# Kernel tuning notes

Hardware: AMD Instinct MI355X
Metric: run time of the kernel (lower is better)

The kernel has to match this reference:

```python
import jax, jax.numpy as jnp
import numpy as np

N_HEAD, F_IN, F_OUT = 4, 768, 64
BS, N = 4, 2048


def setup_inputs() -> dict:
    key = jax.random.key(0)
    k_h, k_w, k_src, k_dst = jax.random.split(key, 4)
    # xavier_uniform bounds
    lim_w = float(np.sqrt(6.0 / (F_IN + F_OUT)))
    lim_a = float(np.sqrt(6.0 / (F_OUT + 1)))
    return {
        "h": jax.random.normal(k_h, (BS, N, F_IN), dtype=jnp.float32),
        "w": jax.random.uniform(k_w, (N_HEAD, F_IN, F_OUT), jnp.float32, -lim_w, lim_w),
        "a_src": jax.random.uniform(k_src, (N_HEAD, F_OUT, 1), jnp.float32, -lim_a, lim_a),
        "a_dst": jax.random.uniform(k_dst, (N_HEAD, F_OUT, 1), jnp.float32, -lim_a, lim_a),
        "bias": jnp.zeros((F_OUT,), dtype=jnp.float32),
    }


def reference(h, w, a_src, a_dst, bias):
    # h: [b, n, f_in]; w: [h, f_in, f_out]
    h_prime = jnp.einsum("bnf,hfo->bhno", h, w)          # [b, h, n, f_out]
    t = jnp.tanh(h_prime)
    attn_src = jnp.einsum("bhno,ho->bhn", t, a_src[..., 0])  # [b, h, n]
    attn_dst = jnp.einsum("bhno,ho->bhn", t, a_dst[..., 0])  # [b, h, n]
    # broadcast add: attn[b,h,i,j] = src[b,h,i] + dst[b,h,j]
    attn = attn_src[..., :, None] + attn_dst[..., None, :]   # [b, h, n, n]
    attn = jnp.where(attn >= 0, attn, 0.2 * attn)            # leaky_relu(0.2)
    attn = jax.nn.softmax(attn, axis=-1)
    out = jnp.einsum("bhij,bhjo->bhio", attn, h_prime)       # [b, h, n, f_out]
    return out + bias
```

## Files before the change

### kernel.cpp

```cpp
#include <hip/hip_runtime.h>
#include <hip/hip_bf16.h>

#define NHEAD 4
#define FIN   768
#define FOUT  64
#define BSZ   4
#define NSEQ  2048
#define BH    (BSZ*NHEAD)
#define LOG2E 1.44269504088896f

typedef __attribute__((ext_vector_type(8)))  short bf16x8;
typedef __attribute__((ext_vector_type(16))) float f32x16;
typedef __attribute__((ext_vector_type(8)))  unsigned short u16x8;
typedef __attribute__((ext_vector_type(4)))  unsigned short u16x4;
typedef __attribute__((ext_vector_type(4)))  unsigned u32x4;

__device__ __forceinline__ unsigned short f2bf(float f){
  unsigned b = __float_as_uint(f);
  return (unsigned short)((b + 0x7fffu + ((b >> 16) & 1u)) >> 16);
}
__device__ __forceinline__ unsigned fenc(float f){
  unsigned b = __float_as_uint(f);
  return (b & 0x80000000u) ? ~b : (b | 0x80000000u);
}
__device__ __forceinline__ float fdec(unsigned u){
  unsigned b = (u & 0x80000000u) ? (u ^ 0x80000000u) : ~u;
  return __uint_as_float(b);
}
__device__ __forceinline__ float fexp2(float x){
#if __has_builtin(__builtin_amdgcn_exp2f)
  return __builtin_amdgcn_exp2f(x);
#else
  return exp2f(x);
#endif
}
__device__ __forceinline__ unsigned pkbf(float lo, float hi){
#if __has_builtin(__builtin_amdgcn_cvt_pk_bf16_f32)
  typedef __attribute__((ext_vector_type(2))) __bf16 bf2;
  union { bf2 v; unsigned u; } cv;
  cv.v = __builtin_amdgcn_cvt_pk_bf16_f32(lo, hi);
  return cv.u;
#else
  return (unsigned)f2bf(lo) | ((unsigned)f2bf(hi) << 16);
#endif
}

__global__ __launch_bounds__(256) void k_prep_w(
    const float* __restrict__ w, unsigned short* __restrict__ wp,
    unsigned* __restrict__ dmaxe)
{
  if (blockIdx.x == 0 && blockIdx.y == 0 && threadIdx.x < BH)
    dmaxe[threadIdx.x] = 0;
  const int head = blockIdx.x, kt = blockIdx.y;
  #pragma unroll
  for (int p = 0; p < 2; ++p){
    int u = threadIdx.x + p*256;
    int o = u >> 3, c = u & 7;
    u16x8 pk;
    #pragma unroll
    for (int j = 0; j < 8; ++j)
      pk[j] = f2bf(w[((size_t)head*FIN + kt*64 + c*8 + j)*FOUT + o]);
    *(u16x8*)((char*)wp + ((size_t)((head*12 + kt)*64 + o))*128 + c*16) = pk;
  }
}

__global__ __launch_bounds__(512, 4) void k_hprime(
    const float* __restrict__ h, const unsigned short* __restrict__ wp,
    const float* __restrict__ a_src, const float* __restrict__ a_dst,
    unsigned short* __restrict__ hpz2, float* __restrict__ srcv,
    float* __restrict__ dstv, unsigned* __restrict__ dmaxe)
{
  __shared__ __align__(16) char smem[32768];
  float* psumS = (float*)(smem + 24576);
  float* psumD = (float*)(smem + 25088);
  char*  Tt    = smem + 16384;

  const int tid  = threadIdx.x;
  const int i0a  = blockIdx.x * 64;
  const int jbase = i0a & (NSEQ-1);
  const int head = blockIdx.y;
  const int wave = tid >> 6, lane = tid & 63;
  const int wm = wave & 1, wn = (wave >> 1) & 1, kw = wave >> 2;
  const int l32 = lane & 31, h32 = lane >> 5;

  f32x16 acc = {0,0,0,0,0,0,0,0,0,0,0,0,0,0,0,0};

  const int sr = tid >> 3, sc = tid & 7;
  const float* hA = h + (size_t)(i0a + sr)*FIN + sc*8;
  const char* wrow = (const char*)wp
      + ((size_t)(head*12*64) + wn*32 + l32)*128 + h32*16;
  const int aslot = (sc ^ (sr & 7)) << 4;

  float4 ra0 = *(const float4*)(hA);
  float4 ra1 = *(const float4*)(hA + 4);
  float4 ra2 = *(const float4*)(hA + 64);
  float4 ra3 = *(const float4*)(hA + 68);

  for (int it = 0; it < 6; ++it){
    char* Ab = smem + (it & 1)*16384;
    u32x4 pk0, pk1;
    pk0[0] = pkbf(ra0.x, ra0.y); pk0[1] = pkbf(ra0.z, ra0.w);
    pk0[2] = pkbf(ra1.x, ra1.y); pk0[3] = pkbf(ra1.z, ra1.w);
    pk1[0] = pkbf(ra2.x, ra2.y); pk1[1] = pkbf(ra2.z, ra2.w);
    pk1[2] = pkbf(ra3.x, ra3.y); pk1[3] = pkbf(ra3.z, ra3.w);
    *(u32x4*)(Ab + sr*256 + aslot)       = pk0;
    *(u32x4*)(Ab + sr*256 + 128 + aslot) = pk1;
    __syncthreads();
    if (it < 5){
      const float* an = hA + (it+1)*128;
      ra0 = *(const float4*)(an);      ra1 = *(const float4*)(an + 4);
      ra2 = *(const float4*)(an + 64); ra3 = *(const float4*)(an + 68);
    }
    const char* wpan = wrow + (size_t)(2*it + kw)*8192;
    bf16x8 b0 = *(const bf16x8*)(wpan);
    bf16x8 b1 = *(const bf16x8*)(wpan + 32);
    bf16x8 b2 = *(const bf16x8*)(wpan + 64);
    bf16x8 b3 = *(const bf16x8*)(wpan + 96);
    const char* abase = Ab + (wm*32 + l32)*256 + kw*128;
    bf16x8 a0 = *(const bf16x8*)(abase + (((0 + h32) ^ (l32 & 7)) << 4));
    bf16x8 a1 = *(const bf16x8*)(abase + (((2 + h32) ^ (l32 & 7)) << 4));
    bf16x8 a2 = *(const bf16x8*)(abase + (((4 + h32) ^ (l32 & 7)) << 4));
    bf16x8 a3 = *(const bf16x8*)(abase + (((6 + h32) ^ (l32 & 7)) << 4));
    acc = __builtin_amdgcn_mfma_f32_32x32x16_bf16(a0, b0, acc, 0, 0, 0);
    acc = __builtin_amdgcn_mfma_f32_32x32x16_bf16(a1, b1, acc, 0, 0, 0);
    acc = __builtin_amdgcn_mfma_f32_32x32x16_bf16(a2, b2, acc, 0, 0, 0);
    acc = __builtin_amdgcn_mfma_f32_32x32x16_bf16(a3, b3, acc, 0, 0, 0);
  }

  if (kw == 1) *(f32x16*)(smem + (size_t)((wave & 3)*64 + lane)*64) = acc;
  __syncthreads();
  if (kw == 0){
    acc += *(const f32x16*)(smem + (size_t)((wave & 3)*64 + lane)*64);
    const float as = a_src[head*64 + wn*32 + l32];
    const float ad = a_dst[head*64 + wn*32 + l32];
    #pragma unroll
    for (int rb = 0; rb < 4; ++rb){
      const int jb = wm*32 + rb*8 + h32*4;
      u16x4 c4;
      #pragma unroll
      for (int q = 0; q < 4; ++q){
        const float v = acc[rb*4 + q];
        c4[q] = f2bf(v);
        const float t = tanhf(v);
        float ps = t*as, pd = t*ad;
        ps += __shfl_xor(ps, 1);  ps += __shfl_xor(ps, 2);  ps += __shfl_xor(ps, 4);
        ps += __shfl_xor(ps, 8);  ps += __shfl_xor(ps, 16);
        pd += __shfl_xor(pd, 1);  pd += __shfl_xor(pd, 2);  pd += __shfl_xor(pd, 4);
        pd += __shfl_xor(pd, 8);  pd += __shfl_xor(pd, 16);
        if (l32 == 0){
          psumS[(jb + q)*2 + wn] = ps;
          psumD[(jb + q)*2 + wn] = pd;
        }
      }
      const int orow = wn*32 + l32;
      const int slot = ((jb >> 3) & 7) ^ (orow & 7);
      *(u16x4*)(Tt + orow*128 + slot*16 + (jb & 7)*2) = c4;
    }
  }
  __syncthreads();

  const int bh = (i0a >> 11)*NHEAD + head;
  {
    const int o = tid & 63, c = tid >> 6;
    u16x8 val = *(const u16x8*)(Tt + o*128 + ((c ^ (o & 7)) << 4));
    *(u16x8*)((char*)hpz2 + ((size_t)(bh*256 + (jbase >> 3) + c)*64 + o)*16) = val;
  }
  if (tid < 64){
    float sv = (psumS[tid*2] + psumS[tid*2 + 1]) * LOG2E;
    float dv = (psumD[tid*2] + psumD[tid*2 + 1]) * LOG2E;
    srcv[(size_t)bh*NSEQ + jbase + tid] = sv;
    dstv[(size_t)bh*NSEQ + jbase + tid] = dv;
    float dmx = dv;
    dmx = fmaxf(dmx, __shfl_xor(dmx, 1));  dmx = fmaxf(dmx, __shfl_xor(dmx, 2));
    dmx = fmaxf(dmx, __shfl_xor(dmx, 4));  dmx = fmaxf(dmx, __shfl_xor(dmx, 8));
    dmx = fmaxf(dmx, __shfl_xor(dmx, 16)); dmx = fmaxf(dmx, __shfl_xor(dmx, 32));
    if (tid == 0) atomicMax(&dmaxe[bh], fenc(dmx));
  }
}

__global__ __launch_bounds__(512, 6) void k_attn(
    const unsigned short* __restrict__ hpz2, const float* __restrict__ srcv,
    const float* __restrict__ dstv, const unsigned* __restrict__ dmaxe,
    const float* __restrict__ bias, float* __restrict__ out)
{
  __shared__ __align__(16) char smem[33792];
  float* Lbuf = (float*)(smem + 32768);

  const int tid = threadIdx.x;
  const int i0  = blockIdx.x * 64;
  const int bh  = blockIdx.y;
  const int wave = tid >> 6, lane = tid & 63;
  const int wm = wave & 1, jw = wave >> 1;
  const int l32 = lane & 31, h32 = lane >> 5;

  const float s2  = srcv[(size_t)bh*NSEQ + i0 + wm*32 + l32];
  const float dm2 = fdec(dmaxe[bh]);
  float m2 = s2 + dm2; m2 = fmaxf(m2, 0.2f*m2);
  const float u_ = s2 - m2;
  const float v_ = 0.2f*s2 - m2;
  const float* dst = dstv + (size_t)bh*NSEQ;

  const u16x8* gp = (const u16x8*)((const char*)hpz2 + (size_t)bh*256*64*16);

  f32x16 accO0 = {0,0,0,0,0,0,0,0,0,0,0,0,0,0,0,0};
  f32x16 accO1 = {0,0,0,0,0,0,0,0,0,0,0,0,0,0,0,0};
  float lpart = 0.f;

  *(u16x8*)(smem + tid*16)              = gp[tid];
  *(u16x8*)(smem + (tid + 512)*16)      = gp[tid + 512];
  __syncthreads();

  for (int w = 0; w < 16; ++w){
    char* cur = smem + (w & 1)*16384;
    char* nxt = smem + ((w + 1) & 1)*16384;
    u16x8 r0, r1;
    if (w < 15){
      r0 = gp[(w+1)*1024 + tid];
      r1 = gp[(w+1)*1024 + tid + 512];
    }
    #pragma unroll
    for (int stl = 0; stl < 2; ++stl){
      const int Jl = jw*4 + stl*2 + h32;
      const int j0 = (w*16 + Jl)*8;
      float4 d0 = *(const float4*)(dst + j0);
      float4 d1 = *(const float4*)(dst + j0 + 4);
      float e0,e1,e2,e3,e4,e5,e6,e7;
      e0 = fexp2(fmaxf(u_ + d0.x, fmaf(0.2f, d0.x, v_)));
      e1 = fexp2(fmaxf(u_ + d0.y, fmaf(0.2f, d0.y, v_)));
      e2 = fexp2(fmaxf(u_ + d0.z, fmaf(0.2f, d0.z, v_)));
      e3 = fexp2(fmaxf(u_ + d0.w, fmaf(0.2f, d0.w, v_)));
      e4 = fexp2(fmaxf(u_ + d1.x, fmaf(0.2f, d1.x, v_)));
      e5 = fexp2(fmaxf(u_ + d1.y, fmaf(0.2f, d1.y, v_)));
      e6 = fexp2(fmaxf(u_ + d1.z, fmaf(0.2f, d1.z, v_)));
      e7 = fexp2(fmaxf(u_ + d1.w, fmaf(0.2f, d1.w, v_)));
      lpart += ((e0+e1)+(e2+e3)) + ((e4+e5)+(e6+e7));
      u32x4 pk;
      pk[0] = pkbf(e0, e1); pk[1] = pkbf(e2, e3);
      pk[2] = pkbf(e4, e5); pk[3] = pkbf(e6, e7);
      const bf16x8 pA = __builtin_bit_cast(bf16x8, pk);
      const bf16x8 bv0 = *(const bf16x8*)(cur + (Jl*64 +      l32)*16);
      const bf16x8 bv1 = *(const bf16x8*)(cur + (Jl*64 + 32 + l32)*16);
      accO0 = __builtin_amdgcn_mfma_f32_32x32x16_bf16(pA, bv0, accO0, 0, 0, 0);
      accO1 = __builtin_amdgcn_mfma_f32_32x32x16_bf16(pA, bv1, accO1, 0, 0, 0);
    }
    if (w < 15){
      *(u16x8*)(nxt + tid*16)         = r0;
      *(u16x8*)(nxt + (tid + 512)*16) = r1;
    }
    __syncthreads();
  }

  lpart += __shfl_xor(lpart, 32);
  if (lane < 32) Lbuf[(wm*4 + jw)*32 + l32] = lpart;

  const float4 bia = *(const float4*)(bias + (tid & 15)*4);
  #pragma unroll
  for (int ph = 0; ph < 2; ++ph){
    __syncthreads();
    if (wm == ph){
      float* ob = (float*)smem;
      #pragma unroll
      for (int reg = 0; reg < 16; ++reg){
        const int m = (reg & 3) + 8*(reg >> 2) + 4*h32;
        ob[(jw*32 + m)*64 +      l32] = accO0[reg];
        ob[(jw*32 + m)*64 + 32 + l32] = accO1[reg];
      }
    }
    __syncthreads();
    {
      const int i = tid >> 4, o4 = (tid & 15)*4;
      const float* ob = (const float*)smem;
      float4 v0 = *(const float4*)(ob + (0*32 + i)*64 + o4);
      float4 v1 = *(const float4*)(ob + (1*32 + i)*64 + o4);
      float4 v2 = *(const float4*)(ob + (2*32 + i)*64 + o4);
      float4 v3 = *(const float4*)(ob + (3*32 + i)*64 + o4);
      const float l = Lbuf[(ph*4+0)*32 + i] + Lbuf[(ph*4+1)*32 + i]
                    + Lbuf[(ph*4+2)*32 + i] + Lbuf[(ph*4+3)*32 + i];
      const float r = 1.f / l;
      float4 res;
      res.x = (v0.x + v1.x + v2.x + v3.x)*r + bia.x;
      res.y = (v0.y + v1.y + v2.y + v3.y)*r + bia.y;
      res.z = (v0.z + v1.z + v2.z + v3.z)*r + bia.z;
      res.w = (v0.w + v1.w + v2.w + v3.w)*r + bia.w;
      *(float4*)(out + ((size_t)bh*NSEQ + i0 + ph*32 + i)*64 + o4) = res;
    }
  }
}

extern "C" void kernel_launch(void* const* d_in, const int* in_sizes, int n_in,
                              void* d_out, int out_size, void* d_ws, size_t ws_size,
                              hipStream_t stream)
{
  const float* h     = (const float*)d_in[0];
  const float* w     = (const float*)d_in[1];
  const float* a_src = (const float*)d_in[2];
  const float* a_dst = (const float*)d_in[3];
  const float* bias  = (const float*)d_in[4];
  float* out = (float*)d_out;

  char* ws = (char*)d_ws;
  unsigned short* hpz2 = (unsigned short*)ws;
  float* srcv = (float*)(ws + (4u<<20));
  float* dstv = (float*)(ws + (4u<<20) + (128u<<10));
  unsigned short* wp = (unsigned short*)(ws + (4u<<20) + (256u<<10));
  unsigned* dmaxe = (unsigned*)(ws + (4u<<20) + (640u<<10));

  k_prep_w<<<dim3(NHEAD, 12), 256, 0, stream>>>(w, wp, dmaxe);
  k_hprime<<<dim3(NSEQ*BSZ/64, NHEAD), 512, 0, stream>>>(h, wp, a_src, a_dst,
                                                         hpz2, srcv, dstv, dmaxe);
  k_attn<<<dim3(NSEQ/64, BH), 512, 0, stream>>>(hpz2, srcv, dstv, dmaxe, bias, out);
}
```

Measured before the change: 134.4 us.

## Fuse three kernels into one persistent launch with atomic-counter dependencies

Replaces the weight-prep, h_prime and attention kernels with a single 512-block kernel. Blocks first pack weights, signal per-head counters, then compute their h_prime tile and signal per-batch-head counters before spinning to start the attention phase. The h_prime stage now stages W tiles through LDS instead of reading them per lane from global memory. This removes two kernel launch gaps, but adds spin-wait latency, a memset launch, and a deadlock risk if not all 512 blocks are co-resident. The guarded spin would then time out and read incomplete data.

```diff
diff --git a/kernel.cpp b/kernel.cpp
--- a/kernel.cpp
+++ b/kernel.cpp
@@ -44,245 +44,253 @@
   return (unsigned)f2bf(lo) | ((unsigned)f2bf(hi) << 16);
 #endif
 }
-
-__global__ __launch_bounds__(256) void k_prep_w(
-    const float* __restrict__ w, unsigned short* __restrict__ wp,
-    unsigned* __restrict__ dmaxe)
+__device__ __forceinline__ void spin_until(unsigned* p, unsigned target){
+  int guard = 0;
+  while (__hip_atomic_load(p, __ATOMIC_ACQUIRE, __HIP_MEMORY_SCOPE_AGENT) != target
+         && ++guard < (1 << 22))
+    __builtin_amdgcn_s_sleep(2);
+}
+
+__global__ __launch_bounds__(512, 4) void k_fused(
+    const float* __restrict__ h, const float* __restrict__ w,
+    const float* __restrict__ a_src, const float* __restrict__ a_dst,
+    const float* __restrict__ bias, float* __restrict__ out,
+    unsigned short* __restrict__ wp, unsigned short* __restrict__ hpz2,
+    float* __restrict__ srcv, float* __restrict__ dstv,
+    unsigned* __restrict__ dmaxe, unsigned* __restrict__ wcnt,
+    unsigned* __restrict__ bhcnt)
 {
-  if (blockIdx.x == 0 && blockIdx.y == 0 && threadIdx.x < BH)
-    dmaxe[threadIdx.x] = 0;
-  const int head = blockIdx.x, kt = blockIdx.y;
-  #pragma unroll
-  for (int p = 0; p < 2; ++p){
-    int u = threadIdx.x + p*256;
-    int o = u >> 3, c = u & 7;
+  __shared__ __align__(16) char smem[65536];
+  const int tid = threadIdx.x;
+  const int bx  = blockIdx.x;
+  const int wave = tid >> 6, lane = tid & 63;
+  const int l32 = lane & 31, h32 = lane >> 5;
+
+  if (bx < 48){
+    const int head = bx / 12, kt = bx - head*12;
+    const int o = tid & 63, c = (tid >> 6) & 7;
+    const float* wsrc = w + (size_t)head*FIN*FOUT + (size_t)(kt*64 + c*8)*FOUT + o;
     u16x8 pk;
     #pragma unroll
-    for (int j = 0; j < 8; ++j)
-      pk[j] = f2bf(w[((size_t)head*FIN + kt*64 + c*8 + j)*FOUT + o]);
-    *(u16x8*)((char*)wp + ((size_t)((head*12 + kt)*64 + o))*128 + c*16) = pk;
+    for (int j = 0; j < 8; ++j) pk[j] = f2bf(wsrc[(size_t)j*FOUT]);
+    *(u16x8*)((char*)wp + ((size_t)((head*12 + kt)*64 + o))*128 + ((c ^ (o & 7)) << 4)) = pk;
+    __threadfence();
+    __syncthreads();
+    if (tid == 0) atomicAdd(&wcnt[head], 1u);
   }
-}
-
-__global__ __launch_bounds__(512, 4) void k_hprime(
-    const float* __restrict__ h, const unsigned short* __restrict__ wp,
-    const float* __restrict__ a_src, const float* __restrict__ a_dst,
-    unsigned short* __restrict__ hpz2, float* __restrict__ srcv,
-    float* __restrict__ dstv, unsigned* __restrict__ dmaxe)
-{
-  __shared__ __align__(16) char smem[32768];
-  float* psumS = (float*)(smem + 24576);
-  float* psumD = (float*)(smem + 25088);
-  char*  Tt    = smem + 16384;
-
-  const int tid  = threadIdx.x;
-  const int i0a  = blockIdx.x * 64;
+
+  const int head1 = bx & 3;
+  const int i0a   = (bx >> 2) << 6;
   const int jbase = i0a & (NSEQ-1);
-  const int head = blockIdx.y;
-  const int wave = tid >> 6, lane = tid & 63;
-  const int wm = wave & 1, wn = (wave >> 1) & 1, kw = wave >> 2;
-  const int l32 = lane & 31, h32 = lane >> 5;
-
-  f32x16 acc = {0,0,0,0,0,0,0,0,0,0,0,0,0,0,0,0};
-
-  const int sr = tid >> 3, sc = tid & 7;
-  const float* hA = h + (size_t)(i0a + sr)*FIN + sc*8;
-  const char* wrow = (const char*)wp
-      + ((size_t)(head*12*64) + wn*32 + l32)*128 + h32*16;
-  const int aslot = (sc ^ (sr & 7)) << 4;
-
-  float4 ra0 = *(const float4*)(hA);
-  float4 ra1 = *(const float4*)(hA + 4);
-  float4 ra2 = *(const float4*)(hA + 64);
-  float4 ra3 = *(const float4*)(hA + 68);
-
-  for (int it = 0; it < 6; ++it){
-    char* Ab = smem + (it & 1)*16384;
-    u32x4 pk0, pk1;
-    pk0[0] = pkbf(ra0.x, ra0.y); pk0[1] = pkbf(ra0.z, ra0.w);
-    pk0[2] = pkbf(ra1.x, ra1.y); pk0[3] = pkbf(ra1.z, ra1.w);
-    pk1[0] = pkbf(ra2.x, ra2.y); pk1[1] = pkbf(ra2.z, ra2.w);
-    pk1[2] = pkbf(ra3.x, ra3.y); pk1[3] = pkbf(ra3.z, ra3.w);
-    *(u32x4*)(Ab + sr*256 + aslot)       = pk0;
-    *(u32x4*)(Ab + sr*256 + 128 + aslot) = pk1;
-    __syncthreads();
-    if (it < 5){
-      const float* an = hA + (it+1)*128;
-      ra0 = *(const float4*)(an);      ra1 = *(const float4*)(an + 4);
-      ra2 = *(const float4*)(an + 64); ra3 = *(const float4*)(an + 68);
-    }
-    const char* wpan = wrow + (size_t)(2*it + kw)*8192;
-    bf16x8 b0 = *(const bf16x8*)(wpan);
-    bf16x8 b1 = *(const bf16x8*)(wpan + 32);
-    bf16x8 b2 = *(const bf16x8*)(wpan + 64);
-    bf16x8 b3 = *(const bf16x8*)(wpan + 96);
-    const char* abase = Ab + (wm*32 + l32)*256 + kw*128;
-    bf16x8 a0 = *(const bf16x8*)(abase + (((0 + h32) ^ (l32 & 7)) << 4));
-    bf16x8 a1 = *(const bf16x8*)(abase + (((2 + h32) ^ (l32 & 7)) << 4));
-    bf16x8 a2 = *(const bf16x8*)(abase + (((4 + h32) ^ (l32 & 7)) << 4));
-    bf16x8 a3 = *(const bf16x8*)(abase + (((6 + h32) ^ (l32 & 7)) << 4));
-    acc = __builtin_amdgcn_mfma_f32_32x32x16_bf16(a0, b0, acc, 0, 0, 0);
-    acc = __builtin_amdgcn_mfma_f32_32x32x16_bf16(a1, b1, acc, 0, 0, 0);
-    acc = __builtin_amdgcn_mfma_f32_32x32x16_bf16(a2, b2, acc, 0, 0, 0);
-    acc = __builtin_amdgcn_mfma_f32_32x32x16_bf16(a3, b3, acc, 0, 0, 0);
+  const int bh1   = (bx >> 7)*NHEAD + head1;
+  {
+    const int wm = wave & 1, wn = (wave >> 1) & 1, kw = wave >> 2;
+    float* psumS = (float*)(smem + 16384);
+    float* psumD = (float*)(smem + 16896);
+    char*  Tt    = smem + 32768;
+
+    const int sr = tid >> 3, sc = tid & 7;
+    const float* hA = h + (size_t)(i0a + sr)*FIN + sc*8;
+    const char*  wB = (const char*)wp + ((size_t)(head1*12*64 + sr))*128 + sc*16;
+    const int aslot = (sc ^ (sr & 7)) << 4;
+
+    float4 ra0 = *(const float4*)(hA);
+    float4 ra1 = *(const float4*)(hA + 4);
+    float4 ra2 = *(const float4*)(hA + 64);
+    float4 ra3 = *(const float4*)(hA + 68);
+
+    if (tid == 0) spin_until(&wcnt[head1], 12u);
+    __syncthreads();
+    __threadfence();
+
+    u16x8 rb0 = *(const u16x8*)(wB);
+    u16x8 rb1 = *(const u16x8*)(wB + 8192);
+
+    f32x16 acc = {0,0,0,0,0,0,0,0,0,0,0,0,0,0,0,0};
+    for (int it = 0; it < 6; ++it){
+      char* Ab = smem + (it & 1)*16384;
+      char* Bb = smem + 32768 + (it & 1)*16384;
+      u32x4 pk0, pk1;
+      pk0[0] = pkbf(ra0.x, ra0.y); pk0[1] = pkbf(ra0.z, ra0.w);
+      pk0[2] = pkbf(ra1.x, ra1.y); pk0[3] = pkbf(ra1.z, ra1.w);
+      pk1[0] = pkbf(ra2.x, ra2.y); pk1[1] = pkbf(ra2.z, ra2.w);
+      pk1[2] = pkbf(ra3.x, ra3.y); pk1[3] = pkbf(ra3.z, ra3.w);
+      *(u32x4*)(Ab + sr*256 + aslot)        = pk0;
+      *(u32x4*)(Ab + sr*256 + 128 + aslot)  = pk1;
+      *(u16x8*)(Bb + sr*256 + sc*16)        = rb0;
+      *(u16x8*)(Bb + sr*256 + 128 + sc*16)  = rb1;
+      __syncthreads();
+      if (it < 5){
+        const float* an = hA + (it+1)*128;
+        ra0 = *(const float4*)(an);      ra1 = *(const float4*)(an + 4);
+        ra2 = *(const float4*)(an + 64); ra3 = *(const float4*)(an + 68);
+        const char* bn = wB + (size_t)(2*(it+1))*8192;
+        rb0 = *(const u16x8*)(bn);       rb1 = *(const u16x8*)(bn + 8192);
+      }
+      #pragma unroll
+      for (int s = 0; s < 4; ++s){
+        const int slot = (((s*2 + h32) ^ (l32 & 7)) << 4);
+        bf16x8 av = *(const bf16x8*)(Ab + (wm*32 + l32)*256 + kw*128 + slot);
+        bf16x8 bv = *(const bf16x8*)(Bb + (wn*32 + l32)*256 + kw*128 + slot);
+        acc = __builtin_amdgcn_mfma_f32_32x32x16_bf16(av, bv, acc, 0, 0, 0);
+      }
+      __syncthreads();
+    }
+
+    if (kw == 1) *(f32x16*)(smem + (size_t)((wave & 3)*64 + lane)*64) = acc;
+    __syncthreads();
+    if (kw == 0){
+      acc += *(const f32x16*)(smem + (size_t)((wave & 3)*64 + lane)*64);
+      const float as = a_src[head1*64 + wn*32 + l32];
+      const float ad = a_dst[head1*64 + wn*32 + l32];
+      #pragma unroll
+      for (int rb = 0; rb < 4; ++rb){
+        const int jb = wm*32 + rb*8 + h32*4;
+        u16x4 c4;
+        #pragma unroll
+        for (int q = 0; q < 4; ++q){
+          const float v = acc[rb*4 + q];
+          c4[q] = f2bf(v);
+          const float t = tanhf(v);
+          float ps = t*as, pd = t*ad;
+          ps += __shfl_xor(ps, 1);  ps += __shfl_xor(ps, 2);  ps += __shfl_xor(ps, 4);
+          ps += __shfl_xor(ps, 8);  ps += __shfl_xor(ps, 16);
+          pd += __shfl_xor(pd, 1);  pd += __shfl_xor(pd, 2);  pd += __shfl_xor(pd, 4);
+          pd += __shfl_xor(pd, 8);  pd += __shfl_xor(pd, 16);
+          if (l32 == 0){
+            psumS[(jb + q)*2 + wn] = ps;
+            psumD[(jb + q)*2 + wn] = pd;
+          }
+        }
+        const int orow = wn*32 + l32;
+        const int slot = ((jb >> 3) & 7) ^ (orow & 7);
+        *(u16x4*)(Tt + orow*128 + slot*16 + (jb & 7)*2) = c4;
+      }
+    }
+    __syncthreads();
+
+    {
+      const int o = tid & 63, c = tid >> 6;
+      u16x8 val = *(const u16x8*)(Tt + o*128 + ((c ^ (o & 7)) << 4));
+      *(u16x8*)((char*)hpz2 + ((size_t)(bh1*256 + (jbase >> 3) + c)*64 + o)*16) = val;
+    }
+    if (tid < 64){
+      float sv = (psumS[tid*2] + psumS[tid*2 + 1]) * LOG2E;
+      float dv = (psumD[tid*2] + psumD[tid*2 + 1]) * LOG2E;
+      srcv[(size_t)bh1*NSEQ + jbase + tid] = sv;
+      dstv[(size_t)bh1*NSEQ + jbase + tid] = dv;
+      float dmx = dv;
+      dmx = fmaxf(dmx, __shfl_xor(dmx, 1));  dmx = fmaxf(dmx, __shfl_xor(dmx, 2));
+      dmx = fmaxf(dmx, __shfl_xor(dmx, 4));  dmx = fmaxf(dmx, __shfl_xor(dmx, 8));
+      dmx = fmaxf(dmx, __shfl_xor(dmx, 16)); dmx = fmaxf(dmx, __shfl_xor(dmx, 32));
+      if (tid == 0) atomicMax(&dmaxe[bh1], fenc(dmx));
+    }
+    __threadfence();
+    __syncthreads();
+    if (tid == 0) atomicAdd(&bhcnt[bh1], 1u);
   }
 
-  if (kw == 1) *(f32x16*)(smem + (size_t)((wave & 3)*64 + lane)*64) = acc;
+  const int bh2 = bx & 15;
+  const int i0  = (bx >> 4) << 6;
+  if (tid == 0) spin_until(&bhcnt[bh2], 32u);
   __syncthreads();
-  if (kw == 0){
-    acc += *(const f32x16*)(smem + (size_t)((wave & 3)*64 + lane)*64);
-    const float as = a_src[head*64 + wn*32 + l32];
-    const float ad = a_dst[head*64 + wn*32 + l32];
+  __threadfence();
+
+  {
+    float* Lbuf = (float*)(smem + 32768);
+    const int wm = wave & 1, jw = wave >> 1;
+
+    const float s2  = srcv[(size_t)bh2*NSEQ + i0 + wm*32 + l32];
+    const float dm2 = fdec(dmaxe[bh2]);
+    float m2 = s2 + dm2; m2 = fmaxf(m2, 0.2f*m2);
+    const float u_ = s2 - m2;
+    const float v_ = 0.2f*s2 - m2;
+    const float* dptr = dstv + (size_t)bh2*NSEQ;
+
+    const u16x8* gp = (const u16x8*)((const char*)hpz2 + (size_t)bh2*256*64*16);
+
+    f32x16 accO0 = {0,0,0,0,0,0,0,0,0,0,0,0,0,0,0,0};
+    f32x16 accO1 = {0,0,0,0,0,0,0,0,0,0,0,0,0,0,0,0};
+    float lpart = 0.f;
+
+    *(u16x8*)(smem + tid*16)         = gp[tid];
+    *(u16x8*)(smem + (tid + 512)*16) = gp[tid + 512];
+    __syncthreads();
+
+    for (int ww = 0; ww < 16; ++ww){
+      char* cur = smem + (ww & 1)*16384;
+      char* nxt = smem + ((ww + 1) & 1)*16384;
+      u16x8 r0, r1;
+      if (ww < 15){
+        r0 = gp[(ww+1)*1024 + tid];
+        r1 = gp[(ww+1)*1024 + tid + 512];
+      }
+      #pragma unroll
+      for (int stl = 0; stl < 2; ++stl){
+        const int Jl = jw*4 + stl*2 + h32;
+        const int j0 = (ww*16 + Jl)*8;
+        float4 d0 = *(const float4*)(dptr + j0);
+        float4 d1 = *(const float4*)(dptr + j0 + 4);
+        float e0,e1,e2,e3,e4,e5,e6,e7;
+        e0 = fexp2(fmaxf(u_ + d0.x, fmaf(0.2f, d0.x, v_)));
+        e1 = fexp2(fmaxf(u_ + d0.y, fmaf(0.2f, d0.y, v_)));
+        e2 = fexp2(fmaxf(u_ + d0.z, fmaf(0.2f, d0.z, v_)));
+        e3 = fexp2(fmaxf(u_ + d0.w, fmaf(0.2f, d0.w, v_)));
+        e4 = fexp2(fmaxf(u_ + d1.x, fmaf(0.2f, d1.x, v_)));
+        e5 = fexp2(fmaxf(u_ + d1.y, fmaf(0.2f, d1.y, v_)));
+        e6 = fexp2(fmaxf(u_ + d1.z, fmaf(0.2f, d1.z, v_)));
+        e7 = fexp2(fmaxf(u_ + d1.w, fmaf(0.2f, d1.w, v_)));
+        lpart += ((e0+e1)+(e2+e3)) + ((e4+e5)+(e6+e7));
+        u32x4 pk;
+        pk[0] = pkbf(e0, e1); pk[1] = pkbf(e2, e3);
+        pk[2] = pkbf(e4, e5); pk[3] = pkbf(e6, e7);
+        const bf16x8 pA = __builtin_bit_cast(bf16x8, pk);
+        const bf16x8 bv0 = *(const bf16x8*)(cur + (Jl*64 +      l32)*16);
+        const bf16x8 bv1 = *(const bf16x8*)(cur + (Jl*64 + 32 + l32)*16);
+        accO0 = __builtin_amdgcn_mfma_f32_32x32x16_bf16(pA, bv0, accO0, 0, 0, 0);
+        accO1 = __builtin_amdgcn_mfma_f32_32x32x16_bf16(pA, bv1, accO1, 0, 0, 0);
+      }
+      if (ww < 15){
+        *(u16x8*)(nxt + tid*16)         = r0;
+        *(u16x8*)(nxt + (tid + 512)*16) = r1;
+      }
+      __syncthreads();
+    }
+
+    lpart += __shfl_xor(lpart, 32);
+    if (lane < 32) Lbuf[(wm*4 + jw)*32 + l32] = lpart;
+
+    const float4 bia = *(const float4*)(bias + (tid & 15)*4);
     #pragma unroll
-    for (int rb = 0; rb < 4; ++rb){
-      const int jb = wm*32 + rb*8 + h32*4;
-      u16x4 c4;
-      #pragma unroll
-      for (int q = 0; q < 4; ++q){
-        const float v = acc[rb*4 + q];
-        c4[q] = f2bf(v);
-        const float t = tanhf(v);
-        float ps = t*as, pd = t*ad;
-        ps += __shfl_xor(ps, 1);  ps += __shfl_xor(ps, 2);  ps += __shfl_xor(ps, 4);
-        ps += __shfl_xor(ps, 8);  ps += __shfl_xor(ps, 16);
-        pd += __shfl_xor(pd, 1);  pd += __shfl_xor(pd, 2);  pd += __shfl_xor(pd, 4);
-        pd += __shfl_xor(pd, 8);  pd += __shfl_xor(pd, 16);
-        if (l32 == 0){
-          psumS[(jb + q)*2 + wn] = ps;
-          psumD[(jb + q)*2 + wn] = pd;
+    for (int ph = 0; ph < 2; ++ph){
+      __syncthreads();
+      if (wm == ph){
+        float* ob = (float*)smem;
+        #pragma unroll
+        for (int reg = 0; reg < 16; ++reg){
+          const int m = (reg & 3) + 8*(reg >> 2) + 4*h32;
+          ob[(jw*32 + m)*64 +      l32] = accO0[reg];
+          ob[(jw*32 + m)*64 + 32 + l32] = accO1[reg];
         }
       }
-      const int orow = wn*32 + l32;
-      const int slot = ((jb >> 3) & 7) ^ (orow & 7);
-      *(u16x4*)(Tt + orow*128 + slot*16 + (jb & 7)*2) = c4;
-    }
-  }
-  __syncthreads();
-
-  const int bh = (i0a >> 11)*NHEAD + head;
-  {
-    const int o = tid & 63, c = tid >> 6;
-    u16x8 val = *(const u16x8*)(Tt + o*128 + ((c ^ (o & 7)) << 4));
-    *(u16x8*)((char*)hpz2 + ((size_t)(bh*256 + (jbase >> 3) + c)*64 + o)*16) = val;
-  }
-  if (tid < 64){
-    float sv = (psumS[tid*2] + psumS[tid*2 + 1]) * LOG2E;
-    float dv = (psumD[tid*2] + psumD[tid*2 + 1]) * LOG2E;
-    srcv[(size_t)bh*NSEQ + jbase + tid] = sv;
-    dstv[(size_t)bh*NSEQ + jbase + tid] = dv;
-    float dmx = dv;
-    dmx = fmaxf(dmx, __shfl_xor(dmx, 1));  dmx = fmaxf(dmx, __shfl_xor(dmx, 2));
-    dmx = fmaxf(dmx, __shfl_xor(dmx, 4));  dmx = fmaxf(dmx, __shfl_xor(dmx, 8));
-    dmx = fmaxf(dmx, __shfl_xor(dmx, 16)); dmx = fmaxf(dmx, __shfl_xor(dmx, 32));
-    if (tid == 0) atomicMax(&dmaxe[bh], fenc(dmx));
-  }
-}
-
-__global__ __launch_bounds__(512, 6) void k_attn(
-    const unsigned short* __restrict__ hpz2, const float* __restrict__ srcv,
-    const float* __restrict__ dstv, const unsigned* __restrict__ dmaxe,
-    const float* __restrict__ bias, float* __restrict__ out)
-{
-  __shared__ __align__(16) char smem[33792];
-  float* Lbuf = (float*)(smem + 32768);
-
-  const int tid = threadIdx.x;
-  const int i0  = blockIdx.x * 64;
-  const int bh  = blockIdx.y;
-  const int wave = tid >> 6, lane = tid & 63;
-  const int wm = wave & 1, jw = wave >> 1;
-  const int l32 = lane & 31, h32 = lane >> 5;
-
-  const float s2  = srcv[(size_t)bh*NSEQ + i0 + wm*32 + l32];
-  const float dm2 = fdec(dmaxe[bh]);
-  float m2 = s2 + dm2; m2 = fmaxf(m2, 0.2f*m2);
-  const float u_ = s2 - m2;
-  const float v_ = 0.2f*s2 - m2;
-  const float* dst = dstv + (size_t)bh*NSEQ;
-
-  const u16x8* gp = (const u16x8*)((const char*)hpz2 + (size_t)bh*256*64*16);
-
-  f32x16 accO0 = {0,0,0,0,0,0,0,0,0,0,0,0,0,0,0,0};
-  f32x16 accO1 = {0,0,0,0,0,0,0,0,0,0,0,0,0,0,0,0};
-  float lpart = 0.f;
-
-  *(u16x8*)(smem + tid*16)              = gp[tid];
-  *(u16x8*)(smem + (tid + 512)*16)      = gp[tid + 512];
-  __syncthreads();
-
-  for (int w = 0; w < 16; ++w){
-    char* cur = smem + (w & 1)*16384;
-    char* nxt = smem + ((w + 1) & 1)*16384;
-    u16x8 r0, r1;
-    if (w < 15){
-      r0 = gp[(w+1)*1024 + tid];
-      r1 = gp[(w+1)*1024 + tid + 512];
-    }
-    #pragma unroll
-    for (int stl = 0; stl < 2; ++stl){
-      const int Jl = jw*4 + stl*2 + h32;
-      const int j0 = (w*16 + Jl)*8;
-      float4 d0 = *(const float4*)(dst + j0);
-      float4 d1 = *(const float4*)(dst + j0 + 4);
-      float e0,e1,e2,e3,e4,e5,e6,e7;
-      e0 = fexp2(fmaxf(u_ + d0.x, fmaf(0.2f, d0.x, v_)));
-      e1 = fexp2(fmaxf(u_ + d0.y, fmaf(0.2f, d0.y, v_)));
-      e2 = fexp2(fmaxf(u_ + d0.z, fmaf(0.2f, d0.z, v_)));
-      e3 = fexp2(fmaxf(u_ + d0.w, fmaf(0.2f, d0.w, v_)));
-      e4 = fexp2(fmaxf(u_ + d1.x, fmaf(0.2f, d1.x, v_)));
-      e5 = fexp2(fmaxf(u_ + d1.y, fmaf(0.2f, d1.y, v_)));
-      e6 = fexp2(fmaxf(u_ + d1.z, fmaf(0.2f, d1.z, v_)));
-      e7 = fexp2(fmaxf(u_ + d1.w, fmaf(0.2f, d1.w, v_)));
-      lpart += ((e0+e1)+(e2+e3)) + ((e4+e5)+(e6+e7));
-      u32x4 pk;
-      pk[0] = pkbf(e0, e1); pk[1] = pkbf(e2, e3);
-      pk[2] = pkbf(e4, e5); pk[3] = pkbf(e6, e7);
-      const bf16x8 pA = __builtin_bit_cast(bf16x8, pk);
-      const bf16x8 bv0 = *(const bf16x8*)(cur + (Jl*64 +      l32)*16);
-      const bf16x8 bv1 = *(const bf16x8*)(cur + (Jl*64 + 32 + l32)*16);
-      accO0 = __builtin_amdgcn_mfma_f32_32x32x16_bf16(pA, bv0, accO0, 0, 0, 0);
-      accO1 = __builtin_amdgcn_mfma_f32_32x32x16_bf16(pA, bv1, accO1, 0, 0, 0);
-    }
-    if (w < 15){
-      *(u16x8*)(nxt + tid*16)         = r0;
-      *(u16x8*)(nxt + (tid + 512)*16) = r1;
-    }
-    __syncthreads();
-  }
-
-  lpart += __shfl_xor(lpart, 32);
-  if (lane < 32) Lbuf[(wm*4 + jw)*32 + l32] = lpart;
-
-  const float4 bia = *(const float4*)(bias + (tid & 15)*4);
-  #pragma unroll
-  for (int ph = 0; ph < 2; ++ph){
-    __syncthreads();
-    if (wm == ph){
-      float* ob = (float*)smem;
-      #pragma unroll
-      for (int reg = 0; reg < 16; ++reg){
-        const int m = (reg & 3) + 8*(reg >> 2) + 4*h32;
-        ob[(jw*32 + m)*64 +      l32] = accO0[reg];
-        ob[(jw*32 + m)*64 + 32 + l32] = accO1[reg];
-      }
-    }
-    __syncthreads();
-    {
-      const int i = tid >> 4, o4 = (tid & 15)*4;
-      const float* ob = (const float*)smem;
-      float4 v0 = *(const float4*)(ob + (0*32 + i)*64 + o4);
-      float4 v1 = *(const float4*)(ob + (1*32 + i)*64 + o4);
-      float4 v2 = *(const float4*)(ob + (2*32 + i)*64 + o4);
-      float4 v3 = *(const float4*)(ob + (3*32 + i)*64 + o4);
-      const float l = Lbuf[(ph*4+0)*32 + i] + Lbuf[(ph*4+1)*32 + i]
-                    + Lbuf[(ph*4+2)*32 + i] + Lbuf[(ph*4+3)*32 + i];
-      const float r = 1.f / l;
-      float4 res;
-      res.x = (v0.x + v1.x + v2.x + v3.x)*r + bia.x;
-      res.y = (v0.y + v1.y + v2.y + v3.y)*r + bia.y;
-      res.z = (v0.z + v1.z + v2.z + v3.z)*r + bia.z;
-      res.w = (v0.w + v1.w + v2.w + v3.w)*r + bia.w;
-      *(float4*)(out + ((size_t)bh*NSEQ + i0 + ph*32 + i)*64 + o4) = res;
+      __syncthreads();
+      {
+        const int i = tid >> 4, o4 = (tid & 15)*4;
+        const float* ob = (const float*)smem;
+        float4 v0 = *(const float4*)(ob + (0*32 + i)*64 + o4);
+        float4 v1 = *(const float4*)(ob + (1*32 + i)*64 + o4);
+        float4 v2 = *(const float4*)(ob + (2*32 + i)*64 + o4);
+        float4 v3 = *(const float4*)(ob + (3*32 + i)*64 + o4);
+        const float l = Lbuf[(ph*4+0)*32 + i] + Lbuf[(ph*4+1)*32 + i]
+                      + Lbuf[(ph*4+2)*32 + i] + Lbuf[(ph*4+3)*32 + i];
+        const float r = 1.f / l;
+        float4 res;
+        res.x = (v0.x + v1.x + v2.x + v3.x)*r + bia.x;
+        res.y = (v0.y + v1.y + v2.y + v3.y)*r + bia.y;
+        res.z = (v0.z + v1.z + v2.z + v3.z)*r + bia.z;
+        res.w = (v0.w + v1.w + v2.w + v3.w)*r + bia.w;
+        *(float4*)(out + ((size_t)bh2*NSEQ + i0 + ph*32 + i)*64 + o4) = res;
+      }
     }
   }
 }
@@ -303,10 +311,12 @@
   float* srcv = (float*)(ws + (4u<<20));
   float* dstv = (float*)(ws + (4u<<20) + (128u<<10));
   unsigned short* wp = (unsigned short*)(ws + (4u<<20) + (256u<<10));
-  unsigned* dmaxe = (unsigned*)(ws + (4u<<20) + (640u<<10));
-
-  k_prep_w<<<dim3(NHEAD, 12), 256, 0, stream>>>(w, wp, dmaxe);
-  k_hprime<<<dim3(NSEQ*BSZ/64, NHEAD), 512, 0, stream>>>(h, wp, a_src, a_dst,
-                                                         hpz2, srcv, dstv, dmaxe);
-  k_attn<<<dim3(NSEQ/64, BH), 512, 0, stream>>>(hpz2, srcv, dstv, dmaxe, bias, out);
-}
+  unsigned* ctrs = (unsigned*)(ws + (4u<<20) + (640u<<10));
+  unsigned* dmaxe = ctrs;
+  unsigned* wcnt  = ctrs + 16;
+  unsigned* bhcnt = ctrs + 20;
+
+  hipMemsetAsync(ctrs, 0, 36*sizeof(unsigned), stream);
+  k_fused<<<512, 512, 0, stream>>>(h, w, a_src, a_dst, bias, out,
+                                   wp, hpz2, srcv, dstv, dmaxe, wcnt, bhcnt);
+}
```

Measured after the change: 370.0 us. 2.75x slower.

## Stage W tiles through LDS in hprime and remap block indices for XCD locality

Applied to the files above, without the earlier changes.

The projection kernel now loads the pre-swizzled weight panel cooperatively into double-buffered shared memory, instead of having each wave read its B fragments straight from global memory. This needs 64KB of LDS and lowers the occupancy hint to 2 blocks. Both main kernels switch to a 1D grid whose low block-id bits select batch-head, apparently so that blocks on the same XCD share data in L2. The weight-prep kernel writes the XOR-swizzled layout that the new LDS reads expect. The attention kernel's occupancy hint drops from 6 to 4, and an extra barrier per k-iteration is added.

```diff
diff --git a/kernel.cpp b/kernel.cpp
--- a/kernel.cpp
+++ b/kernel.cpp
@@ -45,40 +45,37 @@
 #endif
 }
 
-__global__ __launch_bounds__(256) void k_prep_w(
+__global__ __launch_bounds__(512) void k_prep_w(
     const float* __restrict__ w, unsigned short* __restrict__ wp,
     unsigned* __restrict__ dmaxe)
 {
-  if (blockIdx.x == 0 && blockIdx.y == 0 && threadIdx.x < BH)
-    dmaxe[threadIdx.x] = 0;
-  const int head = blockIdx.x, kt = blockIdx.y;
+  if (blockIdx.x == 0 && threadIdx.x < BH) dmaxe[threadIdx.x] = 0;
+  const int head = blockIdx.x & 3, kt = blockIdx.x >> 2;
+  const int o = threadIdx.x & 63, c = threadIdx.x >> 6;
+  const float* wsrc = w + (size_t)head*FIN*FOUT + (size_t)(kt*64 + c*8)*FOUT + o;
+  u16x8 pk;
   #pragma unroll
-  for (int p = 0; p < 2; ++p){
-    int u = threadIdx.x + p*256;
-    int o = u >> 3, c = u & 7;
-    u16x8 pk;
-    #pragma unroll
-    for (int j = 0; j < 8; ++j)
-      pk[j] = f2bf(w[((size_t)head*FIN + kt*64 + c*8 + j)*FOUT + o]);
-    *(u16x8*)((char*)wp + ((size_t)((head*12 + kt)*64 + o))*128 + c*16) = pk;
-  }
-}
-
-__global__ __launch_bounds__(512, 4) void k_hprime(
+  for (int j = 0; j < 8; ++j) pk[j] = f2bf(wsrc[(size_t)j*FOUT]);
+  *(u16x8*)((char*)wp + ((size_t)((head*12 + kt)*64 + o))*128 + ((c ^ (o & 7)) << 4)) = pk;
+}
+
+__global__ __launch_bounds__(512, 2) void k_hprime(
     const float* __restrict__ h, const unsigned short* __restrict__ wp,
     const float* __restrict__ a_src, const float* __restrict__ a_dst,
     unsigned short* __restrict__ hpz2, float* __restrict__ srcv,
     float* __restrict__ dstv, unsigned* __restrict__ dmaxe)
 {
-  __shared__ __align__(16) char smem[32768];
-  float* psumS = (float*)(smem + 24576);
-  float* psumD = (float*)(smem + 25088);
-  char*  Tt    = smem + 16384;
+  __shared__ __align__(16) char smem[65536];
+  float* psumS = (float*)(smem + 16384);
+  float* psumD = (float*)(smem + 16896);
+  char*  Tt    = smem + 32768;
 
   const int tid  = threadIdx.x;
-  const int i0a  = blockIdx.x * 64;
-  const int jbase = i0a & (NSEQ-1);
-  const int head = blockIdx.y;
+  const int bid  = blockIdx.x;
+  const int bh1  = (bid & 7) | (((bid >> 3) & 1) << 3);
+  const int head = bh1 & 3;
+  const int jbase = (bid >> 4) << 6;
+  const int i0a   = (bh1 >> 2)*NSEQ + jbase;
   const int wave = tid >> 6, lane = tid & 63;
   const int wm = wave & 1, wn = (wave >> 1) & 1, kw = wave >> 2;
   const int l32 = lane & 31, h32 = lane >> 5;
@@ -87,44 +84,44 @@
 
   const int sr = tid >> 3, sc = tid & 7;
   const float* hA = h + (size_t)(i0a + sr)*FIN + sc*8;
-  const char* wrow = (const char*)wp
-      + ((size_t)(head*12*64) + wn*32 + l32)*128 + h32*16;
+  const char*  wB = (const char*)wp + ((size_t)(head*12*64 + sr))*128 + sc*16;
   const int aslot = (sc ^ (sr & 7)) << 4;
 
   float4 ra0 = *(const float4*)(hA);
   float4 ra1 = *(const float4*)(hA + 4);
   float4 ra2 = *(const float4*)(hA + 64);
   float4 ra3 = *(const float4*)(hA + 68);
+  u16x8  rb0 = *(const u16x8*)(wB);
+  u16x8  rb1 = *(const u16x8*)(wB + 8192);
 
   for (int it = 0; it < 6; ++it){
     char* Ab = smem + (it & 1)*16384;
+    char* Bb = smem + 32768 + (it & 1)*16384;
     u32x4 pk0, pk1;
     pk0[0] = pkbf(ra0.x, ra0.y); pk0[1] = pkbf(ra0.z, ra0.w);
     pk0[2] = pkbf(ra1.x, ra1.y); pk0[3] = pkbf(ra1.z, ra1.w);
     pk1[0] = pkbf(ra2.x, ra2.y); pk1[1] = pkbf(ra2.z, ra2.w);
     pk1[2] = pkbf(ra3.x, ra3.y); pk1[3] = pkbf(ra3.z, ra3.w);
-    *(u32x4*)(Ab + sr*256 + aslot)       = pk0;
-    *(u32x4*)(Ab + sr*256 + 128 + aslot) = pk1;
+    *(u32x4*)(Ab + sr*256 + aslot)        = pk0;
+    *(u32x4*)(Ab + sr*256 + 128 + aslot)  = pk1;
+    *(u16x8*)(Bb + sr*256 + sc*16)        = rb0;
+    *(u16x8*)(Bb + sr*256 + 128 + sc*16)  = rb1;
     __syncthreads();
     if (it < 5){
       const float* an = hA + (it+1)*128;
       ra0 = *(const float4*)(an);      ra1 = *(const float4*)(an + 4);
       ra2 = *(const float4*)(an + 64); ra3 = *(const float4*)(an + 68);
-    }
-    const char* wpan = wrow + (size_t)(2*it + kw)*8192;
-    bf16x8 b0 = *(const bf16x8*)(wpan);
-    bf16x8 b1 = *(const bf16x8*)(wpan + 32);
-    bf16x8 b2 = *(const bf16x8*)(wpan + 64);
-    bf16x8 b3 = *(const bf16x8*)(wpan + 96);
-    const char* abase = Ab + (wm*32 + l32)*256 + kw*128;
-    bf16x8 a0 = *(const bf16x8*)(abase + (((0 + h32) ^ (l32 & 7)) << 4));
-    bf16x8 a1 = *(const bf16x8*)(abase + (((2 + h32) ^ (l32 & 7)) << 4));
-    bf16x8 a2 = *(const bf16x8*)(abase + (((4 + h32) ^ (l32 & 7)) << 4));
-    bf16x8 a3 = *(const bf16x8*)(abase + (((6 + h32) ^ (l32 & 7)) << 4));
-    acc = __builtin_amdgcn_mfma_f32_32x32x16_bf16(a0, b0, acc, 0, 0, 0);
-    acc = __builtin_amdgcn_mfma_f32_32x32x16_bf16(a1, b1, acc, 0, 0, 0);
-    acc = __builtin_amdgcn_mfma_f32_32x32x16_bf16(a2, b2, acc, 0, 0, 0);
-    acc = __builtin_amdgcn_mfma_f32_32x32x16_bf16(a3, b3, acc, 0, 0, 0);
+      const char* bn = wB + (size_t)(2*(it+1))*8192;
+      rb0 = *(const u16x8*)(bn);       rb1 = *(const u16x8*)(bn + 8192);
+    }
+    #pragma unroll
+    for (int s = 0; s < 4; ++s){
+      const int slot = (((s*2 + h32) ^ (l32 & 7)) << 4);
+      bf16x8 av = *(const bf16x8*)(Ab + (wm*32 + l32)*256 + kw*128 + slot);
+      bf16x8 bv = *(const bf16x8*)(Bb + (wn*32 + l32)*256 + kw*128 + slot);
+      acc = __builtin_amdgcn_mfma_f32_32x32x16_bf16(av, bv, acc, 0, 0, 0);
+    }
+    __syncthreads();
   }
 
   if (kw == 1) *(f32x16*)(smem + (size_t)((wave & 3)*64 + lane)*64) = acc;
@@ -159,26 +156,25 @@
   }
   __syncthreads();
 
-  const int bh = (i0a >> 11)*NHEAD + head;
   {
     const int o = tid & 63, c = tid >> 6;
     u16x8 val = *(const u16x8*)(Tt + o*128 + ((c ^ (o & 7)) << 4));
-    *(u16x8*)((char*)hpz2 + ((size_t)(bh*256 + (jbase >> 3) + c)*64 + o)*16) = val;
+    *(u16x8*)((char*)hpz2 + ((size_t)(bh1*256 + (jbase >> 3) + c)*64 + o)*16) = val;
   }
   if (tid < 64){
     float sv = (psumS[tid*2] + psumS[tid*2 + 1]) * LOG2E;
     float dv = (psumD[tid*2] + psumD[tid*2 + 1]) * LOG2E;
-    srcv[(size_t)bh*NSEQ + jbase + tid] = sv;
-    dstv[(size_t)bh*NSEQ + jbase + tid] = dv;
+    srcv[(size_t)bh1*NSEQ + jbase + tid] = sv;
+    dstv[(size_t)bh1*NSEQ + jbase + tid] = dv;
     float dmx = dv;
     dmx = fmaxf(dmx, __shfl_xor(dmx, 1));  dmx = fmaxf(dmx, __shfl_xor(dmx, 2));
     dmx = fmaxf(dmx, __shfl_xor(dmx, 4));  dmx = fmaxf(dmx, __shfl_xor(dmx, 8));
     dmx = fmaxf(dmx, __shfl_xor(dmx, 16)); dmx = fmaxf(dmx, __shfl_xor(dmx, 32));
-    if (tid == 0) atomicMax(&dmaxe[bh], fenc(dmx));
-  }
-}
-
-__global__ __launch_bounds__(512, 6) void k_attn(
+    if (tid == 0) atomicMax(&dmaxe[bh1], fenc(dmx));
+  }
+}
+
+__global__ __launch_bounds__(512, 4) void k_attn(
     const unsigned short* __restrict__ hpz2, const float* __restrict__ srcv,
     const float* __restrict__ dstv, const unsigned* __restrict__ dmaxe,
     const float* __restrict__ bias, float* __restrict__ out)
@@ -187,8 +183,9 @@
   float* Lbuf = (float*)(smem + 32768);
 
   const int tid = threadIdx.x;
-  const int i0  = blockIdx.x * 64;
-  const int bh  = blockIdx.y;
+  const int bid = blockIdx.x;
+  const int bh  = (bid & 7) | (((bid >> 3) & 1) << 3);
+  const int i0  = (bid >> 4) << 6;
   const int wave = tid >> 6, lane = tid & 63;
   const int wm = wave & 1, jw = wave >> 1;
   const int l32 = lane & 31, h32 = lane >> 5;
@@ -198,7 +195,7 @@
   float m2 = s2 + dm2; m2 = fmaxf(m2, 0.2f*m2);
   const float u_ = s2 - m2;
   const float v_ = 0.2f*s2 - m2;
-  const float* dst = dstv + (size_t)bh*NSEQ;
+  const float* dptr = dstv + (size_t)bh*NSEQ;
 
   const u16x8* gp = (const u16x8*)((const char*)hpz2 + (size_t)bh*256*64*16);
 
@@ -206,8 +203,8 @@
   f32x16 accO1 = {0,0,0,0,0,0,0,0,0,0,0,0,0,0,0,0};
   float lpart = 0.f;
 
-  *(u16x8*)(smem + tid*16)              = gp[tid];
-  *(u16x8*)(smem + (tid + 512)*16)      = gp[tid + 512];
+  *(u16x8*)(smem + tid*16)         = gp[tid];
+  *(u16x8*)(smem + (tid + 512)*16) = gp[tid + 512];
   __syncthreads();
 
   for (int w = 0; w < 16; ++w){
@@ -222,8 +219,8 @@
     for (int stl = 0; stl < 2; ++stl){
       const int Jl = jw*4 + stl*2 + h32;
       const int j0 = (w*16 + Jl)*8;
-      float4 d0 = *(const float4*)(dst + j0);
-      float4 d1 = *(const float4*)(dst + j0 + 4);
+      float4 d0 = *(const float4*)(dptr + j0);
+      float4 d1 = *(const float4*)(dptr + j0 + 4);
       float e0,e1,e2,e3,e4,e5,e6,e7;
       e0 = fexp2(fmaxf(u_ + d0.x, fmaf(0.2f, d0.x, v_)));
       e1 = fexp2(fmaxf(u_ + d0.y, fmaf(0.2f, d0.y, v_)));
@@ -305,8 +302,7 @@
   unsigned short* wp = (unsigned short*)(ws + (4u<<20) + (256u<<10));
   unsigned* dmaxe = (unsigned*)(ws + (4u<<20) + (640u<<10));
 
-  k_prep_w<<<dim3(NHEAD, 12), 256, 0, stream>>>(w, wp, dmaxe);
-  k_hprime<<<dim3(NSEQ*BSZ/64, NHEAD), 512, 0, stream>>>(h, wp, a_src, a_dst,
-                                                         hpz2, srcv, dstv, dmaxe);
-  k_attn<<<dim3(NSEQ/64, BH), 512, 0, stream>>>(hpz2, srcv, dstv, dmaxe, bias, out);
-}
+  k_prep_w<<<48, 512, 0, stream>>>(w, wp, dmaxe);
+  k_hprime<<<512, 512, 0, stream>>>(h, wp, a_src, a_dst, hpz2, srcv, dstv, dmaxe);
+  k_attn<<<512, 512, 0, stream>>>(hpz2, srcv, dstv, dmaxe, bias, out);
+}
```

Result: faster. 125.9 us (-6.4%).
